# Optimization experiments

Hardware: AMD Instinct MI355X
Metric: run time of the kernel (lower is better)

The kernel has to match this reference:

```python
import jax, jax.numpy as jnp
import numpy as np

N_CTX = 4096
D_MODEL = 2048
D_HEAD = 128


def setup_inputs() -> dict:
    key = jax.random.key(0)
    k1, k2, k3, k4 = jax.random.split(key, 4)
    x = jax.random.normal(k1, (N_CTX, D_MODEL), dtype=jnp.float32)
    # torch nn.Linear weights are [out, in]; kept in that layout.
    Wk = jax.random.normal(k2, (D_HEAD, D_MODEL), dtype=jnp.float32) * (1.0 / np.sqrt(D_MODEL))
    Wq = jax.random.normal(k3, (D_HEAD, D_MODEL), dtype=jnp.float32) * (1.0 / np.sqrt(D_MODEL))
    W2 = jax.random.normal(k4, (D_MODEL, D_MODEL), dtype=jnp.float32) * (1.0 / np.sqrt(D_MODEL))
    return {"x": x, "Wk": Wk, "Wq": Wq, "W2": W2}


def reference(x, Wk, Wq, W2):
    # Faithful to the torch module: no 1/sqrt(d_head) scaling, V = x itself.
    n = x.shape[0]
    q = x @ Wq.T                     # [n, d_head]
    k = x @ Wk.T                     # [n, d_head]
    scores = q @ k.T                 # [n, n]
    # causal mask: strictly-upper-triangular entries -> -inf
    causal = jnp.tril(jnp.ones((n, n), dtype=bool))
    scores = jnp.where(causal, scores, -jnp.inf)
    attn = jax.nn.softmax(scores, axis=1)  # [n, n]
    out = attn @ x                   # [n, d_model] (V is the raw input)
    return out @ W2.T                # [n, d_model]
```

## Files before the change

kernel.cpp:

```cpp
#include <hip/hip_runtime.h>

#define NCTX 4096
#define DMODEL 2048
#define DHEAD 128

typedef _Float16 f16;
typedef f16 f16x8 __attribute__((ext_vector_type(8)));
typedef float f32x4 __attribute__((ext_vector_type(4)));
typedef unsigned short u16;
typedef u16 u16x8 __attribute__((ext_vector_type(8)));

__device__ __forceinline__ u16 f2h(float f) {
  union { f16 h; u16 u; } v; v.h = (f16)f; return v.u;
}
__device__ __forceinline__ float h2f(u16 u) {
  union { u16 u; f16 h; } v; v.u = u; return (float)v.h;
}

__device__ __forceinline__ void gl_lds16(const void* g, void* l) {
  __builtin_amdgcn_global_load_lds((const __attribute__((address_space(1))) void*)g,
                                   (__attribute__((address_space(3))) void*)l, 16, 0, 0);
}

__global__ __launch_bounds__(256) void prep_all(const float* __restrict__ x,
                                                const float* __restrict__ Wq,
                                                const float* __restrict__ Wk,
                                                const float* __restrict__ W2,
                                                u16* __restrict__ xf,
                                                u16* __restrict__ Wf, u16* __restrict__ W2f,
                                                u16* __restrict__ XT) {
  __shared__ float tile[64][65];
  int b = blockIdx.x;
  int t = threadIdx.x;
  if (b < 2048) {
    int mb = (b >> 5) * 64, db = (b & 31) * 64;
    int tx = t & 15, ty = t >> 4;
#pragma unroll
    for (int rr = 0; rr < 4; ++rr) {
      int row = rr * 16 + ty;
      float4 v = *(const float4*)(x + (size_t)(mb + row) * DMODEL + db + tx * 4);
      ushort4 h;
      h.x = f2h(v.x); h.y = f2h(v.y); h.z = f2h(v.z); h.w = f2h(v.w);
      size_t gi = ((size_t)(mb + row) * DMODEL + db) / 4 + tx;
      ((ushort4*)xf)[gi] = h;
      tile[row][tx * 4 + 0] = v.x; tile[row][tx * 4 + 1] = v.y;
      tile[row][tx * 4 + 2] = v.z; tile[row][tx * 4 + 3] = v.w;
    }
    __syncthreads();
#pragma unroll
    for (int rr = 0; rr < 4; ++rr) {
      int r = (t >> 4) * 4 + rr;
      int c0 = (t & 15) * 4;
      ushort4 o;
      o.x = f2h(tile[c0 + 0][r]); o.y = f2h(tile[c0 + 1][r]);
      o.z = f2h(tile[c0 + 2][r]); o.w = f2h(tile[c0 + 3][r]);
      *(ushort4*)(XT + (size_t)(db + r) * NCTX + mb + c0) = o;
    }
  } else if (b < 2560) {
    int wk = (b >= 2304);
    int i = (b - (wk ? 2304 : 2048)) * 256 + t;
    const float* W = wk ? Wk : Wq;
    size_t off = wk ? ((size_t)DHEAD * DMODEL / 4) : 0;
    float4 v = ((const float4*)W)[i];
    ushort4 o;
    o.x = f2h(v.x); o.y = f2h(v.y); o.z = f2h(v.z); o.w = f2h(v.w);
    ((ushort4*)Wf)[off + i] = o;
  } else {
    int i = (b - 2560) * 256 + t;
    float4 v = ((const float4*)W2)[i];
    ushort4 o;
    o.x = f2h(v.x); o.y = f2h(v.y); o.z = f2h(v.z); o.w = f2h(v.w);
    ((ushort4*)W2f)[i] = o;
  }
}

__global__ __launch_bounds__(256) void reduce8h(const u16* __restrict__ P,
                                                u16* __restrict__ out, int n8) {
  int i = blockIdx.x * 256 + threadIdx.x;
  if (i >= n8) return;
  float s[8] = {};
#pragma unroll
  for (int z = 0; z < 8; ++z) {
    u16x8 v = ((const u16x8*)P)[(size_t)z * n8 + i];
#pragma unroll
    for (int k = 0; k < 8; ++k) s[k] += h2f(v[k]);
  }
  u16x8 o;
#pragma unroll
  for (int k = 0; k < 8; ++k) o[k] = f2h(s[k]);
  ((u16x8*)out)[i] = o;
}

__global__ __launch_bounds__(256) void reduce_c2(const u16* __restrict__ P,
                                                 u16* __restrict__ out, size_t cs) {
  int row = 2048 + blockIdx.x;
  int t = threadIdx.x;
  size_t base = (size_t)row * DMODEL + t * 8;
  u16x8 a = *(const u16x8*)(P + base);
  u16x8 b = *(const u16x8*)(P + cs + base);
  u16x8 o;
#pragma unroll
  for (int k = 0; k < 8; ++k) o[k] = f2h(h2f(a[k]) + h2f(b[k]));
  *(u16x8*)(out + base) = o;
}

__global__ __launch_bounds__(256) void softmax_wave(const float* __restrict__ S,
                                                    u16* __restrict__ P) {
  int t = threadIdx.x;
  int lane = t & 63, w = t >> 6;
  int b = blockIdx.x;
  int row = (w < 2) ? (2 * b + w) : (4095 - 2 * b - (w - 2));
  const float* srow = S + (size_t)row * NCTX;
  int len = row + 1;
  int jmax = ((row >> 7) + 1) << 7;
  float4 v[16];
  float mx = -3.0e38f;
#pragma unroll
  for (int k = 0; k < 16; ++k) {
    int j = k * 256 + lane * 4;
    if (j < jmax) {
      float4 x = *(const float4*)(srow + j);
      x.x = (j + 0 < len) ? x.x : -3.0e38f;
      x.y = (j + 1 < len) ? x.y : -3.0e38f;
      x.z = (j + 2 < len) ? x.z : -3.0e38f;
      x.w = (j + 3 < len) ? x.w : -3.0e38f;
      v[k] = x;
      mx = fmaxf(mx, fmaxf(fmaxf(x.x, x.y), fmaxf(x.z, x.w)));
    }
  }
#pragma unroll
  for (int o = 32; o > 0; o >>= 1) mx = fmaxf(mx, __shfl_xor(mx, o, 64));
  float sum = 0.f;
#pragma unroll
  for (int k = 0; k < 16; ++k) {
    int j = k * 256 + lane * 4;
    if (j < jmax) {
      float4 x = v[k];
      x.x = (j + 0 < len) ? __expf(x.x - mx) : 0.f;
      x.y = (j + 1 < len) ? __expf(x.y - mx) : 0.f;
      x.z = (j + 2 < len) ? __expf(x.z - mx) : 0.f;
      x.w = (j + 3 < len) ? __expf(x.w - mx) : 0.f;
      v[k] = x;
      sum += x.x + x.y + x.z + x.w;
    }
  }
#pragma unroll
  for (int o = 32; o > 0; o >>= 1) sum += __shfl_xor(sum, o, 64);
  float inv = 1.0f / sum;
  u16* prow = P + (size_t)row * NCTX;
#pragma unroll
  for (int k = 0; k < 16; ++k) {
    int j = k * 256 + lane * 4;
    if (j < jmax) {
      float4 x = v[k];
      ushort4 o4;
      o4.x = f2h(x.x * inv); o4.y = f2h(x.y * inv);
      o4.z = f2h(x.z * inv); o4.w = f2h(x.w * inv);
      *(ushort4*)(prow + j) = o4;
    }
  }
}

__global__ __launch_bounds__(256, 4) void gemm_scores(const u16* __restrict__ A,
                                                      const u16* __restrict__ B,
                                                      float* __restrict__ C) {
  int bm = 31 - blockIdx.x, bn = blockIdx.y;
  if (bn > bm) return;
  __shared__ __align__(16) u16 As[128 * 64];
  __shared__ __align__(16) u16 Bs[128 * 64];
  int t = threadIdx.x;
  int lane = t & 63, w = t >> 6;
  int m0 = bm * 128, n0 = bn * 128;
  int wm = (w >> 1) * 64, wn = (w & 1) * 64;
  int mfrag = lane & 15, quad = lane >> 4;
  int srow = t >> 3, schunk = t & 7;
  int rsw = mfrag & 7;
  f32x4 acc[4][4] = {};
#pragma unroll
  for (int kt = 0; kt < 128; kt += 64) {
#pragma unroll
    for (int p = 0; p < 4; ++p) {
      int row = p * 32 + srow;
      int gsc = schunk ^ (row & 7);
      gl_lds16(A + (size_t)(m0 + row) * 256 + kt + gsc * 8, As + (size_t)(p * 256 + t) * 8);
      gl_lds16(B + (size_t)(n0 + row) * 256 + kt + gsc * 8, Bs + (size_t)(p * 256 + t) * 8);
    }
    __syncthreads();
#pragma unroll
    for (int ks = 0; ks < 2; ++ks) {
      int c0 = ((ks * 4 + quad) ^ rsw) * 8;
      f16x8 af[4], bfr[4];
#pragma unroll
      for (int i = 0; i < 4; ++i)
        af[i] = *(const f16x8*)(As + (wm + i * 16 + mfrag) * 64 + c0);
#pragma unroll
      for (int j = 0; j < 4; ++j)
        bfr[j] = *(const f16x8*)(Bs + (wn + j * 16 + mfrag) * 64 + c0);
#pragma unroll
      for (int i = 0; i < 4; ++i)
#pragma unroll
        for (int j = 0; j < 4; ++j)
          acc[i][j] = __builtin_amdgcn_mfma_f32_16x16x32_f16(af[i], bfr[j], acc[i][j], 0, 0, 0);
    }
    __syncthreads();
  }
#pragma unroll
  for (int i = 0; i < 4; ++i)
#pragma unroll
    for (int j = 0; j < 4; ++j)
#pragma unroll
      for (int rr = 0; rr < 4; ++rr) {
        int row = m0 + wm + i * 16 + quad * 4 + rr;
        int col = n0 + wn + j * 16 + mfrag;
        C[(size_t)row * NCTX + col] = acc[i][j][rr];
      }
}

__global__ __launch_bounds__(256, 4) void gemm_qk(const u16* __restrict__ A,
                                                  const u16* __restrict__ B,
                                                  u16* __restrict__ C) {
  int bm = blockIdx.x, bn = blockIdx.y, kc = blockIdx.z;
  int kStart = kc * 256;
  int kStop = kStart + 256;
  __shared__ __align__(16) u16 As[128 * 64];
  __shared__ __align__(16) u16 Bs[128 * 64];
  int t = threadIdx.x;
  int lane = t & 63, w = t >> 6;
  int m0 = bm * 128, n0 = bn * 128;
  int wm = (w >> 1) * 64, wn = (w & 1) * 64;
  int mfrag = lane & 15, quad = lane >> 4;
  int srow = t >> 3, schunk = t & 7;
  int rsw = mfrag & 7;
  f32x4 acc[4][4] = {};
  for (int kt = kStart; kt < kStop; kt += 64) {
#pragma unroll
    for (int p = 0; p < 4; ++p) {
      int row = p * 32 + srow;
      int gsc = schunk ^ (row & 7);
      gl_lds16(A + (size_t)(m0 + row) * DMODEL + kt + gsc * 8, As + (size_t)(p * 256 + t) * 8);
      gl_lds16(B + (size_t)(n0 + row) * DMODEL + kt + gsc * 8, Bs + (size_t)(p * 256 + t) * 8);
    }
    __syncthreads();
#pragma unroll
    for (int ks = 0; ks < 2; ++ks) {
      int c0 = ((ks * 4 + quad) ^ rsw) * 8;
      f16x8 af[4], bfr[4];
#pragma unroll
      for (int i = 0; i < 4; ++i)
        af[i] = *(const f16x8*)(As + (wm + i * 16 + mfrag) * 64 + c0);
#pragma unroll
      for (int j = 0; j < 4; ++j)
        bfr[j] = *(const f16x8*)(Bs + (wn + j * 16 + mfrag) * 64 + c0);
#pragma unroll
      for (int i = 0; i < 4; ++i)
#pragma unroll
        for (int j = 0; j < 4; ++j)
          acc[i][j] = __builtin_amdgcn_mfma_f32_16x16x32_f16(af[i], bfr[j], acc[i][j], 0, 0, 0);
    }
    __syncthreads();
  }
  u16* Cc = C + (size_t)kc * ((size_t)NCTX * 256);
#pragma unroll
  for (int i = 0; i < 4; ++i)
#pragma unroll
    for (int j = 0; j < 4; ++j)
#pragma unroll
      for (int rr = 0; rr < 4; ++rr) {
        int row = m0 + wm + i * 16 + quad * 4 + rr;
        int col = n0 + wn + j * 16 + mfrag;
        Cc[(size_t)row * 256 + col] = f2h(acc[i][j][rr]);
      }
}

__global__ __launch_bounds__(256, 4) void gemm_f16_p(const u16* __restrict__ A,
                                                     const u16* __restrict__ B,
                                                     float* __restrict__ C,
                                                     int lda, int ldb, int ldc,
                                                     int K) {
  int bm = blockIdx.x, bn = blockIdx.y;
  __shared__ __align__(16) u16 As[128 * 64];
  __shared__ __align__(16) u16 Bs[128 * 64];
  int t = threadIdx.x;
  int lane = t & 63, w = t >> 6;
  int m0 = bm * 128, n0 = bn * 128;
  int wm = (w >> 1) * 64, wn = (w & 1) * 64;
  int mfrag = lane & 15, quad = lane >> 4;
  int srow = t >> 3, schunk = t & 7;
  int rsw = mfrag & 7;
  f32x4 acc[4][4] = {};
  for (int kt = 0; kt < K; kt += 64) {
#pragma unroll
    for (int p = 0; p < 4; ++p) {
      int row = p * 32 + srow;
      int gsc = schunk ^ (row & 7);
      gl_lds16(A + (size_t)(m0 + row) * lda + kt + gsc * 8, As + (size_t)(p * 256 + t) * 8);
      gl_lds16(B + (size_t)(n0 + row) * ldb + kt + gsc * 8, Bs + (size_t)(p * 256 + t) * 8);
    }
    __syncthreads();
#pragma unroll
    for (int ks = 0; ks < 2; ++ks) {
      int c0 = ((ks * 4 + quad) ^ rsw) * 8;
      f16x8 af[4], bfr[4];
#pragma unroll
      for (int i = 0; i < 4; ++i)
        af[i] = *(const f16x8*)(As + (wm + i * 16 + mfrag) * 64 + c0);
#pragma unroll
      for (int j = 0; j < 4; ++j)
        bfr[j] = *(const f16x8*)(Bs + (wn + j * 16 + mfrag) * 64 + c0);
#pragma unroll
      for (int i = 0; i < 4; ++i)
#pragma unroll
        for (int j = 0; j < 4; ++j)
          acc[i][j] = __builtin_amdgcn_mfma_f32_16x16x32_f16(af[i], bfr[j], acc[i][j], 0, 0, 0);
    }
    __syncthreads();
  }
#pragma unroll
  for (int i = 0; i < 4; ++i)
#pragma unroll
    for (int j = 0; j < 4; ++j)
#pragma unroll
      for (int rr = 0; rr < 4; ++rr) {
        int row = m0 + wm + i * 16 + quad * 4 + rr;
        int col = n0 + wn + j * 16 + mfrag;
        C[(size_t)row * ldc + col] = acc[i][j][rr];
      }
}

__global__ __launch_bounds__(256, 4) void gemm_attnx(const u16* __restrict__ A,
                                                     const u16* __restrict__ B,
                                                     u16* __restrict__ C,
                                                     u16* __restrict__ Cf,
                                                     size_t chunkStride) {
  int b = blockIdx.x;
  int s = b >> 8, c = b & 255;
  int r = (s == 0) ? c : (s == 1) ? (511 - c) : (512 + c);
  int bm, bn, kc;
  if (r < 272) {
    bm = 15 + (r >> 4); bn = r & 15; kc = 0;
  } else if (r < 288) {
    bm = 31; bn = r - 272; kc = 1;
  } else {
    int g = (r - 288) >> 5, j = (r - 288) & 31;
    int k = 15 - g;
    if (j < 16) { bm = k - 1; bn = j; kc = 0; }
    else        { bm = 15 + k; bn = j - 16; kc = 1; }
  }
  int kEnd = (bm + 1) * 128;
  if (kEnd > NCTX) kEnd = NCTX;
  int kStart = kc * 2048;
  int kStop = kStart + 2048 < kEnd ? kStart + 2048 : kEnd;
  __shared__ __align__(16) u16 As[128 * 64];
  __shared__ __align__(16) u16 Bs[128 * 64];
  int t = threadIdx.x;
  int lane = t & 63, w = t >> 6;
  int m0 = bm * 128, n0 = bn * 128;
  int wm = (w >> 1) * 64, wn = (w & 1) * 64;
  int mfrag = lane & 15, quad = lane >> 4;
  int srow = t >> 3, schunk = t & 7;
  int rsw = mfrag & 7;
  f32x4 acc[4][4] = {};
  for (int kt = kStart; kt < kStop; kt += 64) {
#pragma unroll
    for (int p = 0; p < 4; ++p) {
      int row = p * 32 + srow;
      int gsc = schunk ^ (row & 7);
      gl_lds16(A + (size_t)(m0 + row) * NCTX + kt + gsc * 8, As + (size_t)(p * 256 + t) * 8);
      gl_lds16(B + (size_t)(n0 + row) * NCTX + kt + gsc * 8, Bs + (size_t)(p * 256 + t) * 8);
    }
    __syncthreads();
#pragma unroll
    for (int ks = 0; ks < 2; ++ks) {
      int c0 = ((ks * 4 + quad) ^ rsw) * 8;
      f16x8 af[4], bfr[4];
#pragma unroll
      for (int i = 0; i < 4; ++i)
        af[i] = *(const f16x8*)(As + (wm + i * 16 + mfrag) * 64 + c0);
#pragma unroll
      for (int j = 0; j < 4; ++j)
        bfr[j] = *(const f16x8*)(Bs + (wn + j * 16 + mfrag) * 64 + c0);
#pragma unroll
      for (int i = 0; i < 4; ++i)
#pragma unroll
        for (int j = 0; j < 4; ++j)
          acc[i][j] = __builtin_amdgcn_mfma_f32_16x16x32_f16(af[i], bfr[j], acc[i][j], 0, 0, 0);
    }
    __syncthreads();
  }
  u16* Cc = (kc == 0 && kEnd <= 2048) ? Cf : (C + (size_t)kc * chunkStride);
#pragma unroll
  for (int i = 0; i < 4; ++i)
#pragma unroll
    for (int j = 0; j < 4; ++j)
#pragma unroll
      for (int rr = 0; rr < 4; ++rr) {
        int row = m0 + wm + i * 16 + quad * 4 + rr;
        int col = n0 + wn + j * 16 + mfrag;
        Cc[(size_t)row * DMODEL + col] = f2h(acc[i][j][rr]);
      }
}

extern "C" void kernel_launch(void* const* d_in, const int* in_sizes, int n_in,
                              void* d_out, int out_size, void* d_ws, size_t ws_size,
                              hipStream_t stream) {
  const float* x  = (const float*)d_in[0];
  const float* Wk = (const float*)d_in[1];
  const float* Wq = (const float*)d_in[2];
  const float* W2 = (const float*)d_in[3];

  char* ws = (char*)d_ws;
  const size_t MB = 1024 * 1024;
  u16*   QKf  = (u16*)  (ws + 0);
  u16*   Wf   = (u16*)  (ws + 2 * MB);
  u16*   xT   = (u16*)  (ws + 3 * MB);
  u16*   W2f  = (u16*)  (ws + 19 * MB);
  u16*   outb = (u16*)  (ws + 27 * MB);
  u16*   attn = (u16*)  (ws + 43 * MB);
  u16*   xf   = (u16*)  (ws + 75 * MB);
  u16*   QKp  = (u16*)  (ws + 107 * MB);
  float* S    = (float*)(ws + 75 * MB);
  u16*   Ph   = (u16*)  (ws + 75 * MB);

  const int QKN8 = NCTX * 256 / 8;
  const size_t CS = (size_t)NCTX * DMODEL;

  prep_all<<<6656, 256, 0, stream>>>(x, Wq, Wk, W2, xf, Wf, W2f, xT);

  gemm_qk<<<dim3(NCTX / 128, 2, 8), 256, 0, stream>>>(xf, Wf, QKp);
  reduce8h<<<(QKN8 + 255) / 256, 256, 0, stream>>>(QKp, QKf, QKN8);

  gemm_scores<<<dim3(32, 32), 256, 0, stream>>>(QKf, QKf + DHEAD, S);
  softmax_wave<<<1024, 256, 0, stream>>>(S, attn);

  gemm_attnx<<<768, 256, 0, stream>>>(attn, xT, Ph, outb, CS);
  reduce_c2<<<2048, 256, 0, stream>>>(Ph, outb, CS);

  gemm_f16_p<<<dim3(NCTX / 128, DMODEL / 128), 256, 0, stream>>>(
      outb, W2f, (float*)d_out, DMODEL, DMODEL, DMODEL, DMODEL);
}
```

Baseline: 224.3 us.

## Reassociate to attn @ (x W2^T) and drop transpose, split-K and reduce

Computes yT = W2·x^T first as a plain GEMM, written transposed as f16, so the final attention product writes fp32 output directly. This reassociation removes the separate x transpose in prep, the split-K attn@x GEMM with its partial-sum reduce kernel, and the final output GEMM. The causal attention GEMM now runs its full K range per tile with a longest-first block order. The trade-off is an extra unmasked 4096x2048x2048 GEMM and less parallelism on long rows, since split-K is gone.

```diff
diff --git a/kernel.cpp b/kernel.cpp
--- a/kernel.cpp
+++ b/kernel.cpp
@@ -27,34 +27,18 @@
                                                 const float* __restrict__ Wk,
                                                 const float* __restrict__ W2,
                                                 u16* __restrict__ xf,
-                                                u16* __restrict__ Wf, u16* __restrict__ W2f,
-                                                u16* __restrict__ XT) {
-  __shared__ float tile[64][65];
+                                                u16* __restrict__ Wf,
+                                                u16* __restrict__ W2f) {
   int b = blockIdx.x;
   int t = threadIdx.x;
   if (b < 2048) {
-    int mb = (b >> 5) * 64, db = (b & 31) * 64;
-    int tx = t & 15, ty = t >> 4;
-#pragma unroll
-    for (int rr = 0; rr < 4; ++rr) {
-      int row = rr * 16 + ty;
-      float4 v = *(const float4*)(x + (size_t)(mb + row) * DMODEL + db + tx * 4);
-      ushort4 h;
-      h.x = f2h(v.x); h.y = f2h(v.y); h.z = f2h(v.z); h.w = f2h(v.w);
-      size_t gi = ((size_t)(mb + row) * DMODEL + db) / 4 + tx;
-      ((ushort4*)xf)[gi] = h;
-      tile[row][tx * 4 + 0] = v.x; tile[row][tx * 4 + 1] = v.y;
-      tile[row][tx * 4 + 2] = v.z; tile[row][tx * 4 + 3] = v.w;
-    }
-    __syncthreads();
-#pragma unroll
-    for (int rr = 0; rr < 4; ++rr) {
-      int r = (t >> 4) * 4 + rr;
-      int c0 = (t & 15) * 4;
+#pragma unroll
+    for (int k = 0; k < 4; ++k) {
+      size_t i = (size_t)b * 1024 + k * 256 + t;
+      float4 v = ((const float4*)x)[i];
       ushort4 o;
-      o.x = f2h(tile[c0 + 0][r]); o.y = f2h(tile[c0 + 1][r]);
-      o.z = f2h(tile[c0 + 2][r]); o.w = f2h(tile[c0 + 3][r]);
-      *(ushort4*)(XT + (size_t)(db + r) * NCTX + mb + c0) = o;
+      o.x = f2h(v.x); o.y = f2h(v.y); o.z = f2h(v.z); o.w = f2h(v.w);
+      ((ushort4*)xf)[i] = o;
     }
   } else if (b < 2560) {
     int wk = (b >= 2304);
@@ -91,19 +75,6 @@
   ((u16x8*)out)[i] = o;
 }
 
-__global__ __launch_bounds__(256) void reduce_c2(const u16* __restrict__ P,
-                                                 u16* __restrict__ out, size_t cs) {
-  int row = 2048 + blockIdx.x;
-  int t = threadIdx.x;
-  size_t base = (size_t)row * DMODEL + t * 8;
-  u16x8 a = *(const u16x8*)(P + base);
-  u16x8 b = *(const u16x8*)(P + cs + base);
-  u16x8 o;
-#pragma unroll
-  for (int k = 0; k < 8; ++k) o[k] = f2h(h2f(a[k]) + h2f(b[k]));
-  *(u16x8*)(out + base) = o;
-}
-
 __global__ __launch_bounds__(256) void softmax_wave(const float* __restrict__ S,
                                                     u16* __restrict__ P) {
   int t = threadIdx.x;
@@ -272,11 +243,9 @@
       }
 }
 
-__global__ __launch_bounds__(256, 4) void gemm_f16_p(const u16* __restrict__ A,
-                                                     const u16* __restrict__ B,
-                                                     float* __restrict__ C,
-                                                     int lda, int ldb, int ldc,
-                                                     int K) {
+__global__ __launch_bounds__(256, 4) void gemm_z(const u16* __restrict__ A,
+                                                 const u16* __restrict__ B,
+                                                 u16* __restrict__ C) {
   int bm = blockIdx.x, bn = blockIdx.y;
   __shared__ __align__(16) u16 As[128 * 64];
   __shared__ __align__(16) u16 Bs[128 * 64];
@@ -288,13 +257,13 @@
   int srow = t >> 3, schunk = t & 7;
   int rsw = mfrag & 7;
   f32x4 acc[4][4] = {};
-  for (int kt = 0; kt < K; kt += 64) {
+  for (int kt = 0; kt < DMODEL; kt += 64) {
 #pragma unroll
     for (int p = 0; p < 4; ++p) {
       int row = p * 32 + srow;
       int gsc = schunk ^ (row & 7);
-      gl_lds16(A + (size_t)(m0 + row) * lda + kt + gsc * 8, As + (size_t)(p * 256 + t) * 8);
-      gl_lds16(B + (size_t)(n0 + row) * ldb + kt + gsc * 8, Bs + (size_t)(p * 256 + t) * 8);
+      gl_lds16(A + (size_t)(m0 + row) * DMODEL + kt + gsc * 8, As + (size_t)(p * 256 + t) * 8);
+      gl_lds16(B + (size_t)(n0 + row) * DMODEL + kt + gsc * 8, Bs + (size_t)(p * 256 + t) * 8);
     }
     __syncthreads();
 #pragma unroll
@@ -323,33 +292,18 @@
       for (int rr = 0; rr < 4; ++rr) {
         int row = m0 + wm + i * 16 + quad * 4 + rr;
         int col = n0 + wn + j * 16 + mfrag;
-        C[(size_t)row * ldc + col] = acc[i][j][rr];
+        C[(size_t)row * NCTX + col] = f2h(acc[i][j][rr]);
       }
 }
 
-__global__ __launch_bounds__(256, 4) void gemm_attnx(const u16* __restrict__ A,
-                                                     const u16* __restrict__ B,
-                                                     u16* __restrict__ C,
-                                                     u16* __restrict__ Cf,
-                                                     size_t chunkStride) {
+__global__ __launch_bounds__(256, 4) void gemm_fin(const u16* __restrict__ A,
+                                                   const u16* __restrict__ B,
+                                                   float* __restrict__ C) {
   int b = blockIdx.x;
-  int s = b >> 8, c = b & 255;
-  int r = (s == 0) ? c : (s == 1) ? (511 - c) : (512 + c);
-  int bm, bn, kc;
-  if (r < 272) {
-    bm = 15 + (r >> 4); bn = r & 15; kc = 0;
-  } else if (r < 288) {
-    bm = 31; bn = r - 272; kc = 1;
-  } else {
-    int g = (r - 288) >> 5, j = (r - 288) & 31;
-    int k = 15 - g;
-    if (j < 16) { bm = k - 1; bn = j; kc = 0; }
-    else        { bm = 15 + k; bn = j - 16; kc = 1; }
-  }
+  int bm, bn;
+  if (b < 256) { bm = 31 - (b >> 4); bn = b & 15; }
+  else         { bm = (b - 256) >> 4; bn = b & 15; }
   int kEnd = (bm + 1) * 128;
-  if (kEnd > NCTX) kEnd = NCTX;
-  int kStart = kc * 2048;
-  int kStop = kStart + 2048 < kEnd ? kStart + 2048 : kEnd;
   __shared__ __align__(16) u16 As[128 * 64];
   __shared__ __align__(16) u16 Bs[128 * 64];
   int t = threadIdx.x;
@@ -360,7 +314,7 @@
   int srow = t >> 3, schunk = t & 7;
   int rsw = mfrag & 7;
   f32x4 acc[4][4] = {};
-  for (int kt = kStart; kt < kStop; kt += 64) {
+  for (int kt = 0; kt < kEnd; kt += 64) {
 #pragma unroll
     for (int p = 0; p < 4; ++p) {
       int row = p * 32 + srow;
@@ -387,7 +341,6 @@
     }
     __syncthreads();
   }
-  u16* Cc = (kc == 0 && kEnd <= 2048) ? Cf : (C + (size_t)kc * chunkStride);
 #pragma unroll
   for (int i = 0; i < 4; ++i)
 #pragma unroll
@@ -396,7 +349,7 @@
       for (int rr = 0; rr < 4; ++rr) {
         int row = m0 + wm + i * 16 + quad * 4 + rr;
         int col = n0 + wn + j * 16 + mfrag;
-        Cc[(size_t)row * DMODEL + col] = f2h(acc[i][j][rr]);
+        C[(size_t)row * DMODEL + col] = acc[i][j][rr];
       }
 }
 
@@ -412,29 +365,24 @@
   const size_t MB = 1024 * 1024;
   u16*   QKf  = (u16*)  (ws + 0);
   u16*   Wf   = (u16*)  (ws + 2 * MB);
-  u16*   xT   = (u16*)  (ws + 3 * MB);
-  u16*   W2f  = (u16*)  (ws + 19 * MB);
-  u16*   outb = (u16*)  (ws + 27 * MB);
+  u16*   W2f  = (u16*)  (ws + 3 * MB);
+  u16*   xf   = (u16*)  (ws + 11 * MB);
+  u16*   yT   = (u16*)  (ws + 27 * MB);
   u16*   attn = (u16*)  (ws + 43 * MB);
-  u16*   xf   = (u16*)  (ws + 75 * MB);
-  u16*   QKp  = (u16*)  (ws + 107 * MB);
+  u16*   QKp  = (u16*)  (ws + 75 * MB);
   float* S    = (float*)(ws + 75 * MB);
-  u16*   Ph   = (u16*)  (ws + 75 * MB);
 
   const int QKN8 = NCTX * 256 / 8;
-  const size_t CS = (size_t)NCTX * DMODEL;
-
-  prep_all<<<6656, 256, 0, stream>>>(x, Wq, Wk, W2, xf, Wf, W2f, xT);
+
+  prep_all<<<6656, 256, 0, stream>>>(x, Wq, Wk, W2, xf, Wf, W2f);
 
   gemm_qk<<<dim3(NCTX / 128, 2, 8), 256, 0, stream>>>(xf, Wf, QKp);
   reduce8h<<<(QKN8 + 255) / 256, 256, 0, stream>>>(QKp, QKf, QKN8);
 
+  gemm_z<<<dim3(DMODEL / 128, NCTX / 128), 256, 0, stream>>>(W2f, xf, yT);
+
   gemm_scores<<<dim3(32, 32), 256, 0, stream>>>(QKf, QKf + DHEAD, S);
   softmax_wave<<<1024, 256, 0, stream>>>(S, attn);
 
-  gemm_attnx<<<768, 256, 0, stream>>>(attn, xT, Ph, outb, CS);
-  reduce_c2<<<2048, 256, 0, stream>>>(Ph, outb, CS);
-
-  gemm_f16_p<<<dim3(NCTX / 128, DMODEL / 128), 256, 0, stream>>>(
-      outb, W2f, (float*)d_out, DMODEL, DMODEL, DMODEL, DMODEL);
-}
+  gemm_fin<<<512, 256, 0, stream>>>(attn, yT, (float*)d_out);
+}
```

Measured after the change: 242.5 us. +8.1%, slower.
